# Kernel tuning notes

Hardware: AMD Instinct MI355X
Metric: run time of the kernel (lower is better)

Reference implementation:

```python
import jax, jax.numpy as jnp
import numpy as np

TOP_K = 6
N_EXPERTS = 64
ALPHA = 1e-3


def setup_inputs() -> dict:
    key = jax.random.key(0)
    k1, k2 = jax.random.split(key)
    bsz, seq_len, h = 4, 4096, 2048
    hidden_states = jax.random.normal(k1, (bsz, seq_len, h), dtype=jnp.float32)
    # kaiming_uniform_(a=sqrt(5)) on [E, h] -> bound = 1/sqrt(h)
    bound = 1.0 / np.sqrt(h)
    weight = jax.random.uniform(k2, (N_EXPERTS, h), dtype=jnp.float32, minval=-bound, maxval=bound)
    return {"hidden_states": hidden_states, "weight": weight}


def reference(hidden_states, weight):
    bsz, seq_len, h = hidden_states.shape
    E = weight.shape[0]
    x = hidden_states.reshape(-1, h)                      # [T, h], T = bsz*seq_len
    logits = jnp.einsum('th,eh->te', x, weight)           # router linear (no bias)
    scores = jax.nn.softmax(logits, axis=-1)              # [T, E]
    topk_weight, topk_idx = jax.lax.top_k(scores, TOP_K)  # [T, K]
    # norm_topk_prob renormalization
    topk_weight = topk_weight / (jnp.sum(topk_weight, axis=-1, keepdims=True) + 1e-20)
    # seq_aux auxiliary load-balancing loss (training path)
    idx_b = topk_idx.reshape(bsz, seq_len * TOP_K)        # [B, S*K]
    ce = jnp.sum(jax.nn.one_hot(idx_b, E, dtype=scores.dtype), axis=1)  # [B, E] counts
    ce = ce / (seq_len * TOP_K / E)
    mean_scores = scores.reshape(bsz, seq_len, E).mean(axis=1)          # [B, E]
    aux_loss = jnp.mean(jnp.sum(ce * mean_scores, axis=1)) * ALPHA
    return topk_idx, topk_weight, aux_loss
```

## Files before the change

kernel.cpp:

```cpp
#include <hip/hip_runtime.h>
#include <math.h>

#pragma clang fp contract(off)

#define T_TOKENS 16384
#define HDIM 2048
#define NEXP 64
#define TOPK 6
#define SEQ 4096
#define TPB 32
#define KC 64
#define WS 68
#define XS 68
#define LGS 65
#define PS 65

__device__ __forceinline__ void np_upd(const float4& w0, const float4& w1,
                                       const float4& w2, const float4& w3,
                                       const float4& x0, const float4& x1,
                                       const float4& x2, const float4& x3,
                                       float acc[4])
{
    acc[0] = w0.x*x0.x + (w1.x*x1.x + (w2.x*x2.x + (w3.x*x3.x + acc[0])));
    acc[1] = w0.y*x0.y + (w1.y*x1.y + (w2.y*x2.y + (w3.y*x3.y + acc[1])));
    acc[2] = w0.z*x0.z + (w1.z*x1.z + (w2.z*x2.z + (w3.z*x3.z + acc[2])));
    acc[3] = w0.w*x0.w + (w1.w*x1.w + (w2.w*x2.w + (w3.w*x3.w + acc[3])));
}

__global__ __launch_bounds__(256) void moe_gate_main(
    const float* __restrict__ x, const float* __restrict__ wgt,
    float* __restrict__ out, float* __restrict__ gacc)
{
    __shared__ float w_lds[NEXP * WS];
    __shared__ float x_lds[TPB * XS];
    __shared__ float lg[TPB * LGS];
    __shared__ float probs[TPB * PS];
    __shared__ float psum[4 * NEXP];
    __shared__ int   cnt[NEXP];

    const int tid  = threadIdx.x;
    const int bid  = blockIdx.x;
    const int tb   = bid * TPB;
    const int b    = tb / SEQ;

    const int lane = tid & 63;
    const int wv   = tid >> 6;
    const int le   = lane & 15;
    const int g    = lane >> 4;
    const int trow0 = wv * 8 + g * 2;

    float acc[4][2][4];
    #pragma unroll
    for (int j = 0; j < 4; ++j)
        #pragma unroll
        for (int t = 0; t < 2; ++t)
            #pragma unroll
            for (int l = 0; l < 4; ++l) acc[j][t][l] = 0.f;

    for (int c = 0; c < HDIM / KC; ++c) {
        const int k0 = c * KC;
        #pragma unroll
        for (int i = 0; i < 4; ++i) {
            int idx = i * 256 + tid;
            int e = idx >> 4, c4 = idx & 15;
            float4 v = *reinterpret_cast<const float4*>(&wgt[e * HDIM + k0 + c4 * 4]);
            *reinterpret_cast<float4*>(&w_lds[e * WS + c4 * 4]) = v;
        }
        #pragma unroll
        for (int i = 0; i < 2; ++i) {
            int idx = i * 256 + tid;
            int t = idx >> 4, c4 = idx & 15;
            float4 v = *reinterpret_cast<const float4*>(&x[(size_t)(tb + t) * HDIM + k0 + c4 * 4]);
            *reinterpret_cast<float4*>(&x_lds[t * XS + c4 * 4]) = v;
        }
        __syncthreads();

        #pragma unroll
        for (int b16 = 0; b16 < 4; ++b16) {
            const int kb = b16 * 16;
            float4 xa[2][4];
            #pragma unroll
            for (int tt = 0; tt < 2; ++tt)
                #pragma unroll
                for (int j = 0; j < 4; ++j)
                    xa[tt][j] = *reinterpret_cast<const float4*>(&x_lds[(trow0 + tt) * XS + kb + j * 4]);
            #pragma unroll
            for (int je = 0; je < 4; ++je) {
                const float* wr = &w_lds[(le + 16 * je) * WS + kb];
                float4 w0 = *reinterpret_cast<const float4*>(wr);
                float4 w1 = *reinterpret_cast<const float4*>(wr + 4);
                float4 w2 = *reinterpret_cast<const float4*>(wr + 8);
                float4 w3 = *reinterpret_cast<const float4*>(wr + 12);
                np_upd(w0, w1, w2, w3, xa[0][0], xa[0][1], xa[0][2], xa[0][3], acc[je][0]);
                np_upd(w0, w1, w2, w3, xa[1][0], xa[1][1], xa[1][2], xa[1][3], acc[je][1]);
            }
        }
        __syncthreads();
    }

    #pragma unroll
    for (int je = 0; je < 4; ++je)
        #pragma unroll
        for (int tt = 0; tt < 2; ++tt) {
            float v = (acc[je][tt][0] + acc[je][tt][1]) + (acc[je][tt][2] + acc[je][tt][3]);
            lg[(trow0 + tt) * LGS + le + 16 * je] = v;
        }
    if (tid < NEXP) cnt[tid] = 0;
    __syncthreads();

    if (tid < TPB) {
        const int t = tid;
        float mx = lg[t * LGS];
        for (int e = 1; e < NEXP; ++e) { float v = lg[t * LGS + e]; if (v > mx) mx = v; }
        for (int e = 0; e < NEXP; ++e)
            probs[t * PS + e] = expf(lg[t * LGS + e] - mx);
        float r[8];
        #pragma unroll
        for (int j = 0; j < 8; ++j) r[j] = probs[t * PS + j];
        for (int i = 8; i < 64; i += 8)
            #pragma unroll
            for (int j = 0; j < 8; ++j) r[j] += probs[t * PS + i + j];
        float S = ((r[0] + r[1]) + (r[2] + r[3])) + ((r[4] + r[5]) + (r[6] + r[7]));
        for (int e = 0; e < NEXP; ++e) probs[t * PS + e] = probs[t * PS + e] / S;
    }
    __syncthreads();

    {
        const int e = tid & 63, q = tid >> 6;
        float s = 0.f;
        for (int t = q * 8; t < q * 8 + 8; ++t) s += probs[t * PS + e];
        psum[q * 64 + e] = s;
    }
    __syncthreads();

    if (tid < TPB) {
        const int t = tid;
        const int gt = tb + t;
        float pv[TOPK]; int pi[TOPK];
        for (int r = 0; r < TOPK; ++r) {
            float bv = -1.f; int be = 0;
            for (int e = 0; e < NEXP; ++e) {
                float v = probs[t * PS + e];
                if (v > bv) { bv = v; be = e; }
            }
            probs[t * PS + be] = -1.f;
            pv[r] = bv; pi[r] = be;
            atomicAdd(&cnt[be], 1);
        }
        float wsum = pv[0];
        #pragma unroll
        for (int r = 1; r < TOPK; ++r) wsum += pv[r];
        wsum += 1e-20f;
        #pragma unroll
        for (int r = 0; r < TOPK; ++r) {
            out[(size_t)gt * TOPK + r] = (float)pi[r];
            out[(size_t)T_TOKENS * TOPK + (size_t)gt * TOPK + r] = pv[r] / wsum;
        }
    } else if (tid >= 64 && tid < 128) {
        const int e = tid - 64;
        float s = psum[e] + psum[64 + e] + psum[128 + e] + psum[192 + e];
        atomicAdd(&gacc[b * 64 + e], s);
    }
    __syncthreads();
    if (tid < NEXP) {
        atomicAdd(&gacc[256 + b * 64 + tid], (float)cnt[tid]);
    }
}

__global__ __launch_bounds__(256) void moe_gate_aux(
    const float* __restrict__ gacc, float* __restrict__ out)
{
    __shared__ float red[4];
    const int tid = threadIdx.x;
    float v = gacc[256 + tid] * gacc[tid];
    #pragma unroll
    for (int o = 32; o > 0; o >>= 1) v += __shfl_down(v, o, 64);
    if ((tid & 63) == 0) red[tid >> 6] = v;
    __syncthreads();
    if (tid == 0) {
        float tot = red[0] + red[1] + red[2] + red[3];
        const float scale = (64.0f / (4096.0f * 6.0f)) / 4096.0f;
        out[2 * T_TOKENS * TOPK] = 1e-3f * (tot * scale) * 0.25f;
    }
}

extern "C" void kernel_launch(void* const* d_in, const int* in_sizes, int n_in,
                              void* d_out, int out_size, void* d_ws, size_t ws_size,
                              hipStream_t stream) {
    const float* x   = (const float*)d_in[0];
    const float* wgt = (const float*)d_in[1];
    float* out  = (float*)d_out;
    float* gacc = (float*)d_ws;

    hipMemsetAsync(d_ws, 0, 512 * sizeof(float), stream);
    moe_gate_main<<<T_TOKENS / TPB, 256, 0, stream>>>(x, wgt, out, gacc);
    moe_gate_aux<<<1, 256, 0, stream>>>(gacc, out);
}
```

Measured before the change: 309.3 us.

## Use packed FP32 math with register-tiled tokens and direct global x loads

Blocks shrink to 128 threads, and each thread now computes 8 tokens × 4 experts using v_pk_mul/v_pk_add packed FP32 inline asm. The K dimension is split into two interleaved halves that are combined through LDS at the end. Activations are loaded straight from global memory as float2 into registers, with no LDS staging, and the logits/probs buffers reuse the weight LDS. The aim is more FLOPs per LDS load and double-rate packed FP32. The costs are higher register pressure, uncoalesced 8-byte global loads of x, and a changed summation order.

```diff
diff --git a/kernel.cpp b/kernel.cpp
--- a/kernel.cpp
+++ b/kernel.cpp
@@ -2,6 +2,8 @@
 #include <math.h>
 
 #pragma clang fp contract(off)
+
+typedef float f32x2 __attribute__((ext_vector_type(2)));
 
 #define T_TOKENS 16384
 #define HDIM 2048
@@ -9,103 +11,104 @@
 #define TOPK 6
 #define SEQ 4096
 #define TPB 32
+#define NTHR 128
 #define KC 64
 #define WS 68
-#define XS 68
 #define LGS 65
-#define PS 65
-
-__device__ __forceinline__ void np_upd(const float4& w0, const float4& w1,
-                                       const float4& w2, const float4& w3,
-                                       const float4& x0, const float4& x1,
-                                       const float4& x2, const float4& x3,
-                                       float acc[4])
-{
-    acc[0] = w0.x*x0.x + (w1.x*x1.x + (w2.x*x2.x + (w3.x*x3.x + acc[0])));
-    acc[1] = w0.y*x0.y + (w1.y*x1.y + (w2.y*x2.y + (w3.y*x3.y + acc[1])));
-    acc[2] = w0.z*x0.z + (w1.z*x1.z + (w2.z*x2.z + (w3.z*x3.z + acc[2])));
-    acc[3] = w0.w*x0.w + (w1.w*x1.w + (w2.w*x2.w + (w3.w*x3.w + acc[3])));
-}
-
-__global__ __launch_bounds__(256) void moe_gate_main(
+
+__device__ __forceinline__ void pk_macc(f32x2 &acc, f32x2 a, f32x2 b) {
+    f32x2 p, r;
+    asm("v_pk_mul_f32 %0, %1, %2" : "=v"(p) : "v"(a), "v"(b));
+    asm("v_pk_add_f32 %0, %1, %2" : "=v"(r) : "v"(p), "v"(acc));
+    acc = r;
+}
+
+__global__ __launch_bounds__(NTHR, 2) void moe_gate_main(
     const float* __restrict__ x, const float* __restrict__ wgt,
     float* __restrict__ out, float* __restrict__ gacc)
 {
     __shared__ float w_lds[NEXP * WS];
-    __shared__ float x_lds[TPB * XS];
-    __shared__ float lg[TPB * LGS];
-    __shared__ float probs[TPB * PS];
-    __shared__ float psum[4 * NEXP];
+    __shared__ float psum[2 * NEXP];
     __shared__ int   cnt[NEXP];
 
-    const int tid  = threadIdx.x;
-    const int bid  = blockIdx.x;
-    const int tb   = bid * TPB;
-    const int b    = tb / SEQ;
-
-    const int lane = tid & 63;
-    const int wv   = tid >> 6;
-    const int le   = lane & 15;
-    const int g    = lane >> 4;
-    const int trow0 = wv * 8 + g * 2;
-
-    float acc[4][2][4];
+    const int tid = threadIdx.x;
+    const int bid = blockIdx.x;
+    const int tb  = bid * TPB;
+    const int b   = tb >> 12;
+
+    const int le = tid & 15;
+    const int h  = (tid >> 4) & 1;
+    const int tg = tid >> 5;
+    const int t0 = tg * 8;
+
+    f32x2 acc[4][8];
     #pragma unroll
-    for (int j = 0; j < 4; ++j)
-        #pragma unroll
-        for (int t = 0; t < 2; ++t)
-            #pragma unroll
-            for (int l = 0; l < 4; ++l) acc[j][t][l] = 0.f;
+    for (int je = 0; je < 4; ++je)
+        #pragma unroll
+        for (int tt = 0; tt < 8; ++tt) { acc[je][tt].x = 0.f; acc[je][tt].y = 0.f; }
+
+    const float* xbase = x + (size_t)(tb + t0) * HDIM + 2 * h;
 
     for (int c = 0; c < HDIM / KC; ++c) {
         const int k0 = c * KC;
         #pragma unroll
-        for (int i = 0; i < 4; ++i) {
-            int idx = i * 256 + tid;
+        for (int i = 0; i < 8; ++i) {
+            int idx = i * NTHR + tid;
             int e = idx >> 4, c4 = idx & 15;
             float4 v = *reinterpret_cast<const float4*>(&wgt[e * HDIM + k0 + c4 * 4]);
             *reinterpret_cast<float4*>(&w_lds[e * WS + c4 * 4]) = v;
         }
-        #pragma unroll
-        for (int i = 0; i < 2; ++i) {
-            int idx = i * 256 + tid;
-            int t = idx >> 4, c4 = idx & 15;
-            float4 v = *reinterpret_cast<const float4*>(&x[(size_t)(tb + t) * HDIM + k0 + c4 * 4]);
-            *reinterpret_cast<float4*>(&x_lds[t * XS + c4 * 4]) = v;
-        }
         __syncthreads();
 
         #pragma unroll
         for (int b16 = 0; b16 < 4; ++b16) {
-            const int kb = b16 * 16;
-            float4 xa[2][4];
-            #pragma unroll
-            for (int tt = 0; tt < 2; ++tt)
+            const int lb = b16 * 16;
+            f32x2 xa[8][4];
+            #pragma unroll
+            for (int tt = 0; tt < 8; ++tt)
                 #pragma unroll
                 for (int j = 0; j < 4; ++j)
-                    xa[tt][j] = *reinterpret_cast<const float4*>(&x_lds[(trow0 + tt) * XS + kb + j * 4]);
-            #pragma unroll
-            for (int je = 0; je < 4; ++je) {
-                const float* wr = &w_lds[(le + 16 * je) * WS + kb];
-                float4 w0 = *reinterpret_cast<const float4*>(wr);
-                float4 w1 = *reinterpret_cast<const float4*>(wr + 4);
-                float4 w2 = *reinterpret_cast<const float4*>(wr + 8);
-                float4 w3 = *reinterpret_cast<const float4*>(wr + 12);
-                np_upd(w0, w1, w2, w3, xa[0][0], xa[0][1], xa[0][2], xa[0][3], acc[je][0]);
-                np_upd(w0, w1, w2, w3, xa[1][0], xa[1][1], xa[1][2], xa[1][3], acc[je][1]);
+                    xa[tt][j] = *reinterpret_cast<const f32x2*>(
+                        &xbase[(size_t)tt * HDIM + k0 + lb + j * 4]);
+            #pragma unroll
+            for (int j = 3; j >= 0; --j) {
+                f32x2 wf[4];
+                #pragma unroll
+                for (int je = 0; je < 4; ++je)
+                    wf[je] = *reinterpret_cast<const f32x2*>(
+                        &w_lds[(le + 16 * je) * WS + lb + j * 4 + 2 * h]);
+                #pragma unroll
+                for (int je = 0; je < 4; ++je)
+                    #pragma unroll
+                    for (int tt = 0; tt < 8; ++tt)
+                        pk_macc(acc[je][tt], wf[je], xa[tt][j]);
             }
         }
         __syncthreads();
     }
 
-    #pragma unroll
-    for (int je = 0; je < 4; ++je)
-        #pragma unroll
-        for (int tt = 0; tt < 2; ++tt) {
-            float v = (acc[je][tt][0] + acc[je][tt][1]) + (acc[je][tt][2] + acc[je][tt][3]);
-            lg[(trow0 + tt) * LGS + le + 16 * je] = v;
-        }
+    float* lg    = w_lds;
+    float* part1 = w_lds + TPB * LGS;
+
+    if (h == 1) {
+        #pragma unroll
+        for (int je = 0; je < 4; ++je)
+            #pragma unroll
+            for (int tt = 0; tt < 8; ++tt)
+                part1[(t0 + tt) * LGS + le + 16 * je] = acc[je][tt].x + acc[je][tt].y;
+    }
     if (tid < NEXP) cnt[tid] = 0;
+    __syncthreads();
+    if (h == 0) {
+        #pragma unroll
+        for (int je = 0; je < 4; ++je)
+            #pragma unroll
+            for (int tt = 0; tt < 8; ++tt) {
+                float p0 = acc[je][tt].x + acc[je][tt].y;
+                lg[(t0 + tt) * LGS + le + 16 * je] =
+                    p0 + part1[(t0 + tt) * LGS + le + 16 * je];
+            }
+    }
     __syncthreads();
 
     if (tid < TPB) {
@@ -113,22 +116,22 @@
         float mx = lg[t * LGS];
         for (int e = 1; e < NEXP; ++e) { float v = lg[t * LGS + e]; if (v > mx) mx = v; }
         for (int e = 0; e < NEXP; ++e)
-            probs[t * PS + e] = expf(lg[t * LGS + e] - mx);
+            lg[t * LGS + e] = expf(lg[t * LGS + e] - mx);
         float r[8];
         #pragma unroll
-        for (int j = 0; j < 8; ++j) r[j] = probs[t * PS + j];
+        for (int j = 0; j < 8; ++j) r[j] = lg[t * LGS + j];
         for (int i = 8; i < 64; i += 8)
             #pragma unroll
-            for (int j = 0; j < 8; ++j) r[j] += probs[t * PS + i + j];
+            for (int j = 0; j < 8; ++j) r[j] += lg[t * LGS + i + j];
         float S = ((r[0] + r[1]) + (r[2] + r[3])) + ((r[4] + r[5]) + (r[6] + r[7]));
-        for (int e = 0; e < NEXP; ++e) probs[t * PS + e] = probs[t * PS + e] / S;
+        for (int e = 0; e < NEXP; ++e) lg[t * LGS + e] = lg[t * LGS + e] / S;
     }
     __syncthreads();
 
     {
         const int e = tid & 63, q = tid >> 6;
         float s = 0.f;
-        for (int t = q * 8; t < q * 8 + 8; ++t) s += probs[t * PS + e];
+        for (int t = q * 16; t < q * 16 + 16; ++t) s += lg[t * LGS + e];
         psum[q * 64 + e] = s;
     }
     __syncthreads();
@@ -140,10 +143,10 @@
         for (int r = 0; r < TOPK; ++r) {
             float bv = -1.f; int be = 0;
             for (int e = 0; e < NEXP; ++e) {
-                float v = probs[t * PS + e];
+                float v = lg[t * LGS + e];
                 if (v > bv) { bv = v; be = e; }
             }
-            probs[t * PS + be] = -1.f;
+            lg[t * LGS + be] = -1.f;
             pv[r] = bv; pi[r] = be;
             atomicAdd(&cnt[be], 1);
         }
@@ -158,8 +161,7 @@
         }
     } else if (tid >= 64 && tid < 128) {
         const int e = tid - 64;
-        float s = psum[e] + psum[64 + e] + psum[128 + e] + psum[192 + e];
-        atomicAdd(&gacc[b * 64 + e], s);
+        atomicAdd(&gacc[b * 64 + e], psum[e] + psum[64 + e]);
     }
     __syncthreads();
     if (tid < NEXP) {
@@ -193,6 +195,6 @@
     float* gacc = (float*)d_ws;
 
     hipMemsetAsync(d_ws, 0, 512 * sizeof(float), stream);
-    moe_gate_main<<<T_TOKENS / TPB, 256, 0, stream>>>(x, wgt, out, gacc);
+    moe_gate_main<<<T_TOKENS / TPB, NTHR, 0, stream>>>(x, wgt, out, gacc);
     moe_gate_aux<<<1, 256, 0, stream>>>(gacc, out);
 }
```

Measured after the change: 679.1 us. 2.2x slower.

## Load token rows directly into registers with software prefetch instead of LDS staging

Applied to the files above, without the earlier changes.

Removes the x tile staging through shared memory. Each thread now reads its two token rows straight from global memory into registers and prefetches the next 16-element slice while computing the current one. Only the weight tile still goes through LDS, with the barrier moved to the top of the chunk loop, and launch bounds now request 2 blocks per CU. This cuts LDS traffic and one barrier per chunk, at the cost of less coalesced global reads (16 threads read the same x row) and more live registers.

```diff
diff --git a/kernel.cpp b/kernel.cpp
--- a/kernel.cpp
+++ b/kernel.cpp
@@ -9,11 +9,10 @@
 #define TOPK 6
 #define SEQ 4096
 #define TPB 32
+#define NTHR 256
 #define KC 64
 #define WS 68
-#define XS 68
 #define LGS 65
-#define PS 65
 
 __device__ __forceinline__ void np_upd(const float4& w0, const float4& w1,
                                        const float4& w2, const float4& w3,
@@ -27,75 +26,81 @@
     acc[3] = w0.w*x0.w + (w1.w*x1.w + (w2.w*x2.w + (w3.w*x3.w + acc[3])));
 }
 
-__global__ __launch_bounds__(256) void moe_gate_main(
+__global__ __launch_bounds__(NTHR, 2) void moe_gate_main(
     const float* __restrict__ x, const float* __restrict__ wgt,
     float* __restrict__ out, float* __restrict__ gacc)
 {
     __shared__ float w_lds[NEXP * WS];
-    __shared__ float x_lds[TPB * XS];
     __shared__ float lg[TPB * LGS];
-    __shared__ float probs[TPB * PS];
+    __shared__ float probs[TPB * LGS];
     __shared__ float psum[4 * NEXP];
     __shared__ int   cnt[NEXP];
 
-    const int tid  = threadIdx.x;
-    const int bid  = blockIdx.x;
-    const int tb   = bid * TPB;
-    const int b    = tb / SEQ;
-
-    const int lane = tid & 63;
-    const int wv   = tid >> 6;
-    const int le   = lane & 15;
-    const int g    = lane >> 4;
-    const int trow0 = wv * 8 + g * 2;
+    const int tid = threadIdx.x;
+    const int bid = blockIdx.x;
+    const int tb  = bid * TPB;
+    const int b   = tb >> 12;
+
+    const int le    = tid & 15;
+    const int grp   = tid >> 4;
+    const int trow0 = grp * 2;
+
+    const float* xp0 = x + (size_t)(tb + trow0) * HDIM;
+    const float* xp1 = xp0 + HDIM;
 
     float acc[4][2][4];
     #pragma unroll
-    for (int j = 0; j < 4; ++j)
-        #pragma unroll
-        for (int t = 0; t < 2; ++t)
-            #pragma unroll
-            for (int l = 0; l < 4; ++l) acc[j][t][l] = 0.f;
+    for (int je = 0; je < 4; ++je)
+        #pragma unroll
+        for (int tt = 0; tt < 2; ++tt)
+            #pragma unroll
+            for (int l = 0; l < 4; ++l) acc[je][tt][l] = 0.f;
+
+    float4 xc[2][4], xn[2][4];
+    #pragma unroll
+    for (int j = 0; j < 4; ++j) {
+        xc[0][j] = *reinterpret_cast<const float4*>(xp0 + 4 * j);
+        xc[1][j] = *reinterpret_cast<const float4*>(xp1 + 4 * j);
+    }
 
     for (int c = 0; c < HDIM / KC; ++c) {
         const int k0 = c * KC;
+        __syncthreads();
         #pragma unroll
         for (int i = 0; i < 4; ++i) {
-            int idx = i * 256 + tid;
+            int idx = i * NTHR + tid;
             int e = idx >> 4, c4 = idx & 15;
             float4 v = *reinterpret_cast<const float4*>(&wgt[e * HDIM + k0 + c4 * 4]);
             *reinterpret_cast<float4*>(&w_lds[e * WS + c4 * 4]) = v;
         }
-        #pragma unroll
-        for (int i = 0; i < 2; ++i) {
-            int idx = i * 256 + tid;
-            int t = idx >> 4, c4 = idx & 15;
-            float4 v = *reinterpret_cast<const float4*>(&x[(size_t)(tb + t) * HDIM + k0 + c4 * 4]);
-            *reinterpret_cast<float4*>(&x_lds[t * XS + c4 * 4]) = v;
-        }
         __syncthreads();
 
         #pragma unroll
         for (int b16 = 0; b16 < 4; ++b16) {
-            const int kb = b16 * 16;
-            float4 xa[2][4];
-            #pragma unroll
-            for (int tt = 0; tt < 2; ++tt)
+            const int kb = k0 + b16 * 16;
+            if (kb + 16 < HDIM) {
                 #pragma unroll
-                for (int j = 0; j < 4; ++j)
-                    xa[tt][j] = *reinterpret_cast<const float4*>(&x_lds[(trow0 + tt) * XS + kb + j * 4]);
+                for (int j = 0; j < 4; ++j) {
+                    xn[0][j] = *reinterpret_cast<const float4*>(xp0 + kb + 16 + 4 * j);
+                    xn[1][j] = *reinterpret_cast<const float4*>(xp1 + kb + 16 + 4 * j);
+                }
+            }
+            const int lb = b16 * 16;
             #pragma unroll
             for (int je = 0; je < 4; ++je) {
-                const float* wr = &w_lds[(le + 16 * je) * WS + kb];
+                const float* wr = &w_lds[(le + 16 * je) * WS + lb];
                 float4 w0 = *reinterpret_cast<const float4*>(wr);
                 float4 w1 = *reinterpret_cast<const float4*>(wr + 4);
                 float4 w2 = *reinterpret_cast<const float4*>(wr + 8);
                 float4 w3 = *reinterpret_cast<const float4*>(wr + 12);
-                np_upd(w0, w1, w2, w3, xa[0][0], xa[0][1], xa[0][2], xa[0][3], acc[je][0]);
-                np_upd(w0, w1, w2, w3, xa[1][0], xa[1][1], xa[1][2], xa[1][3], acc[je][1]);
+                np_upd(w0, w1, w2, w3, xc[0][0], xc[0][1], xc[0][2], xc[0][3], acc[je][0]);
+                np_upd(w0, w1, w2, w3, xc[1][0], xc[1][1], xc[1][2], xc[1][3], acc[je][1]);
             }
-        }
-        __syncthreads();
+            #pragma unroll
+            for (int t = 0; t < 2; ++t)
+                #pragma unroll
+                for (int j = 0; j < 4; ++j) xc[t][j] = xn[t][j];
+        }
     }
 
     #pragma unroll
@@ -113,22 +118,22 @@
         float mx = lg[t * LGS];
         for (int e = 1; e < NEXP; ++e) { float v = lg[t * LGS + e]; if (v > mx) mx = v; }
         for (int e = 0; e < NEXP; ++e)
-            probs[t * PS + e] = expf(lg[t * LGS + e] - mx);
+            probs[t * LGS + e] = expf(lg[t * LGS + e] - mx);
         float r[8];
         #pragma unroll
-        for (int j = 0; j < 8; ++j) r[j] = probs[t * PS + j];
+        for (int j = 0; j < 8; ++j) r[j] = probs[t * LGS + j];
         for (int i = 8; i < 64; i += 8)
             #pragma unroll
-            for (int j = 0; j < 8; ++j) r[j] += probs[t * PS + i + j];
+            for (int j = 0; j < 8; ++j) r[j] += probs[t * LGS + i + j];
         float S = ((r[0] + r[1]) + (r[2] + r[3])) + ((r[4] + r[5]) + (r[6] + r[7]));
-        for (int e = 0; e < NEXP; ++e) probs[t * PS + e] = probs[t * PS + e] / S;
+        for (int e = 0; e < NEXP; ++e) probs[t * LGS + e] = probs[t * LGS + e] / S;
     }
     __syncthreads();
 
     {
         const int e = tid & 63, q = tid >> 6;
         float s = 0.f;
-        for (int t = q * 8; t < q * 8 + 8; ++t) s += probs[t * PS + e];
+        for (int t = q * 8; t < q * 8 + 8; ++t) s += probs[t * LGS + e];
         psum[q * 64 + e] = s;
     }
     __syncthreads();
@@ -140,10 +145,10 @@
         for (int r = 0; r < TOPK; ++r) {
             float bv = -1.f; int be = 0;
             for (int e = 0; e < NEXP; ++e) {
-                float v = probs[t * PS + e];
+                float v = probs[t * LGS + e];
                 if (v > bv) { bv = v; be = e; }
             }
-            probs[t * PS + be] = -1.f;
+            probs[t * LGS + be] = -1.f;
             pv[r] = bv; pi[r] = be;
             atomicAdd(&cnt[be], 1);
         }
@@ -193,6 +198,6 @@
     float* gacc = (float*)d_ws;
 
     hipMemsetAsync(d_ws, 0, 512 * sizeof(float), stream);
-    moe_gate_main<<<T_TOKENS / TPB, 256, 0, stream>>>(x, wgt, out, gacc);
+    moe_gate_main<<<T_TOKENS / TPB, NTHR, 0, stream>>>(x, wgt, out, gacc);
     moe_gate_aux<<<1, 256, 0, stream>>>(gacc, out);
 }
```

After: 1.183 ms. 282% more time.
